# Performance work log

Hardware: AMD Instinct MI355X
Metric: run time of the kernel (lower is better)

The kernel has to match this reference:

```python
import jax, jax.numpy as jnp
import numpy as np

LN_EPS = 1e-5
ADJ_EPS = 1e-8
LRELU_SLOPE = 0.2


def _layernorm(x, g, b):
    m = x.mean(-1, keepdims=True)
    v = ((x - m) ** 2).mean(-1, keepdims=True)
    return (x - m) / jnp.sqrt(v + LN_EPS) * g + b


def _gat(h, adj, W, a, dim_head, proj=None):
    # h: [B,N,Din]; adj: [B,N,N]; W: [Din, H*dh]; a: [H, 2*dh]
    B, N, _ = h.shape
    H = a.shape[0]
    ht = (h @ W).reshape(B, N, H, dim_head)          # [B,N,H,dh]
    # additive attention: a . [h_i || h_j] splits into two rank-1 terms,
    # so we never materialize the O(B N^2 H 2dh) concat tensor.
    ei = jnp.einsum('bnhd,hd->bnh', ht, a[:, :dim_head])
    ej = jnp.einsum('bnhd,hd->bnh', ht, a[:, dim_head:])
    e = ei[:, :, None, :] + ej[:, None, :, :]        # [B,N,N,H]
    e = jnp.where(e > 0, e, LRELU_SLOPE * e)         # leaky relu(0.2)
    mask = (adj > 0)[..., None]                      # [B,N,N,1]
    e = jnp.where(mask, e, -jnp.inf)
    alpha = jax.nn.softmax(e, axis=2)                # softmax over neighbors m
    hagg = jnp.einsum('bnmh,bmhd->bnhd', alpha, ht)  # [B,N,H,dh]
    out = hagg.reshape(B, N, -1)
    if proj is not None:
        Wp, bp = proj
        out = out @ Wp + bp
    return out


def setup_inputs() -> dict:
    key = jax.random.key(0)
    ks = jax.random.split(key, 24)
    B, N, DN, DH, H = 64, 360, 360, 256, 8
    s = 0.05
    nrm = lambda k, sh, sc=s: (jax.random.normal(k, sh) * sc).astype(jnp.float32)
    return {
        'mind_matrix': jax.random.uniform(ks[0], (B, N, N), dtype=jnp.float32),
        'roi_features_img': jax.random.normal(ks[1], (B, N, DH), dtype=jnp.float32),
        'group_prior': jax.random.uniform(ks[2], (N, N), dtype=jnp.float32),
        'Wnp': nrm(ks[3], (DN, DH)), 'bnp': jnp.zeros((DH,), jnp.float32),
        'Wrf': nrm(ks[4], (2 * DH, DH)), 'brf': jnp.zeros((DH,), jnp.float32),
        'ln_g': jnp.ones((DH,), jnp.float32), 'ln_b': jnp.zeros((DH,), jnp.float32),
        'Wp1': nrm(ks[5], (1, 32)), 'bp1': jnp.zeros((32,), jnp.float32),
        'Wp2': nrm(ks[6], (32, 1)), 'bp2': jnp.zeros((1,), jnp.float32),
        'gatW0': nrm(ks[7], (DH, DH)), 'gata0': nrm(ks[8], (H, 64), 1.0),
        'gatW1': nrm(ks[9], (DH, DH)), 'gata1': nrm(ks[10], (H, 64), 1.0),
        'gatW2': nrm(ks[11], (DH, H * DH)), 'gata2': nrm(ks[12], (H, 2 * DH), 1.0),
        'projW': nrm(ks[13], (H * DH, DH)), 'projb': jnp.zeros((DH,), jnp.float32),
        'Wr1': nrm(ks[14], (DH, DH)), 'br1': jnp.zeros((DH,), jnp.float32),
        'Wr2': nrm(ks[15], (DH, DH)), 'br2': jnp.zeros((DH,), jnp.float32),
    }


def reference(mind_matrix, roi_features_img, group_prior,
              Wnp, bnp, Wrf, brf, ln_g, ln_b,
              Wp1, bp1, Wp2, bp2,
              gatW0, gata0, gatW1, gata1, gatW2, gata2, projW, projb,
              Wr1, br1, Wr2, br2):
    # node feature fusion
    node_mind = mind_matrix @ Wnp + bnp                       # [B,N,256]
    nf = jnp.concatenate([node_mind, roi_features_img], -1) @ Wrf + brf
    nf = jax.nn.gelu(_layernorm(nf, ln_g, ln_b), approximate=False)
    # prior-modulated adjacency (tau = 1.0)
    adj_base = jnp.exp(-mind_matrix)                          # [B,N,N]
    pm = jax.nn.relu(group_prior[..., None] @ Wp1 + bp1)      # [N,N,32]
    pm = jax.nn.sigmoid(pm @ Wp2 + bp2)[..., 0]               # [N,N]
    adj_mod = adj_base * (1.0 + pm)[None]
    adj_norm = adj_mod / (adj_mod.sum(-1, keepdims=True) + ADJ_EPS)
    # hierarchical GAT (dropout inactive at eval)
    h = _gat(nf, adj_norm, gatW0, gata0, 32)
    h = _gat(h, adj_norm, gatW1, gata1, 32)
    h = _gat(h, adj_norm, gatW2, gata2, 256, (projW, projb))  # concat=False layer
    # attention readout
    node_attention = jax.nn.softmax(jnp.linalg.norm(h, axis=-1), axis=-1)  # [B,N]
    ge = jnp.einsum('bn,bnd->bd', node_attention, h)
    ge = jax.nn.gelu(ge @ Wr1 + br1, approximate=False) @ Wr2 + br2
    return ge, h, node_attention
```

## Files before the change

### kernel.cpp

```cpp
#include <hip/hip_runtime.h>
#include <hip/hip_bf16.h>
#include <math.h>


#define B_ 64
#define N_ 360
#define D_ 256
#define H_ 8
#define ROWS_ (B_ * N_)
#define CHUNK01 30
#define SCPAD 964

__device__ __forceinline__ float gelu_f(float x) {
    return 0.5f * x * (1.f + erff(x * 0.70710678118654752440f));
}

__global__ __launch_bounds__(256) void gemm_tiled(
    const float* __restrict__ A1, const float* __restrict__ B1, int K1, int lda1, int ldb1,
    const float* __restrict__ A2, const float* __restrict__ B2, int K2, int lda2, int ldb2,
    const float* __restrict__ bias, float* __restrict__ C, int M, int N, int ldc,
    size_t sA, size_t sB, size_t sC)
{
    __shared__ float As[2][32][132];
    __shared__ float Bs[2][32][64];
    const int tid = threadIdx.x;
    const int z = blockIdx.z;
    const int bm = blockIdx.y * 128;
    const int bn = blockIdx.x * 64;
    const int tr = (tid >> 4) * 8;
    const int tc = (tid & 15) * 4;
    const int lar = tid >> 3;
    const int lak = (tid & 7) * 4;
    const int lbk = tid >> 4;
    const int lbc = (tid & 15) * 4;

    float acc[8][4] = {};
    float4 rA[4], rB[2];

    for (int pass = 0; pass < 2; ++pass) {
        const float* Ab = pass ? A2 : A1;
        const float* Bb = pass ? B2 : B1;
        if (Ab == nullptr) continue;
        const float* A  = Ab + (pass ? (size_t)0 : (size_t)z * sA);
        const float* Bm = Bb + (pass ? (size_t)0 : (size_t)z * sB);
        const int K   = pass ? K2 : K1;
        const int lda = pass ? lda2 : lda1;
        const int ldb = pass ? ldb2 : ldb1;
        const int S = (K + 31) >> 5;

        auto loadA = [&](int s) {
            const int k0 = s << 5;
            #pragma unroll
            for (int j = 0; j < 4; ++j) {
                const int gr = bm + lar + j * 32;
                const int gk = k0 + lak;
                float4 v; v.x = v.y = v.z = v.w = 0.f;
                if (gr < M) {
                    if (gk + 3 < K) {
                        v = *(const float4*)&A[(size_t)gr * lda + gk];
                    } else {
                        float t0 = 0.f, t1 = 0.f, t2 = 0.f, t3 = 0.f;
                        if (gk + 0 < K) t0 = A[(size_t)gr * lda + gk + 0];
                        if (gk + 1 < K) t1 = A[(size_t)gr * lda + gk + 1];
                        if (gk + 2 < K) t2 = A[(size_t)gr * lda + gk + 2];
                        if (gk + 3 < K) t3 = A[(size_t)gr * lda + gk + 3];
                        v.x = t0; v.y = t1; v.z = t2; v.w = t3;
                    }
                }
                rA[j] = v;
            }
        };
        auto loadB = [&](int s) {
            const int k0 = s << 5;
            #pragma unroll
            for (int j = 0; j < 2; ++j) {
                const int gk = k0 + lbk + j * 16;
                float4 v; v.x = v.y = v.z = v.w = 0.f;
                if (gk < K) v = *(const float4*)&Bm[(size_t)gk * ldb + bn + lbc];
                rB[j] = v;
            }
        };
        auto storeA = [&](int buf) {
            #pragma unroll
            for (int j = 0; j < 4; ++j) {
                const int row = lar + j * 32;
                As[buf][lak + 0][row] = rA[j].x;
                As[buf][lak + 1][row] = rA[j].y;
                As[buf][lak + 2][row] = rA[j].z;
                As[buf][lak + 3][row] = rA[j].w;
            }
        };
        auto storeB = [&](int buf) {
            #pragma unroll
            for (int j = 0; j < 2; ++j)
                *(float4*)&Bs[buf][lbk + j * 16][lbc] = rB[j];
        };

        loadA(0); loadB(0);
        storeA(0); storeB(0);
        __syncthreads();
        for (int s = 0; s < S; ++s) {
            const int cur = s & 1;
            if (s + 1 < S) { loadA(s + 1); loadB(s + 1); }
            #pragma unroll
            for (int k = 0; k < 32; ++k) {
                const float4 a0 = *(const float4*)&As[cur][k][tr];
                const float4 a1 = *(const float4*)&As[cur][k][tr + 4];
                const float4 bv = *(const float4*)&Bs[cur][k][tc];
                const float av[8] = {a0.x, a0.y, a0.z, a0.w, a1.x, a1.y, a1.z, a1.w};
                const float bb[4] = {bv.x, bv.y, bv.z, bv.w};
                #pragma unroll
                for (int i = 0; i < 8; ++i)
                    #pragma unroll
                    for (int j = 0; j < 4; ++j)
                        acc[i][j] += av[i] * bb[j];
            }
            if (s + 1 < S) { storeA(cur ^ 1); storeB(cur ^ 1); }
            __syncthreads();
        }
    }

    float4 bz; bz.x = bz.y = bz.z = bz.w = 0.f;
    if (bias) bz = *(const float4*)&bias[bn + tc];
    float* Cz = C + (size_t)z * sC;
    #pragma unroll
    for (int i = 0; i < 8; ++i) {
        const int r = bm + tr + i;
        if (r < M) {
            float4 o;
            o.x = acc[i][0] + bz.x;
            o.y = acc[i][1] + bz.y;
            o.z = acc[i][2] + bz.z;
            o.w = acc[i][3] + bz.w;
            *(float4*)&Cz[(size_t)r * ldc + bn + tc] = o;
        }
    }
}

__global__ __launch_bounds__(256) void biascomb_kernel(
    const float* __restrict__ bnp, const float* __restrict__ Wrf,
    const float* __restrict__ brf, float* __restrict__ bcomb)
{
    int c = threadIdx.x;
    float acc = brf[c];
    for (int k = 0; k < 256; ++k) acc += bnp[k] * Wrf[k * 256 + c];
    bcomb[c] = acc;
}

__global__ __launch_bounds__(256) void uv_kernel(
    const float* __restrict__ gatW2, const float* __restrict__ a2,
    float* __restrict__ u, float* __restrict__ v)
{
    const int h = blockIdx.x;
    const int i = threadIdx.x;
    const float* wrow = gatW2 + (size_t)i * 2048 + h * 256;
    const float* ai = a2 + h * 512;
    float su = 0.f, sv = 0.f;
    for (int j = 0; j < 256; ++j) {
        float w = wrow[j];
        su += w * ai[j];
        sv += w * ai[256 + j];
    }
    u[h * 256 + i] = su;
    v[h * 256 + i] = sv;
}

__global__ __launch_bounds__(64) void ln_gelu_kernel(
    float* __restrict__ x, const float* __restrict__ g, const float* __restrict__ b)
{
    const size_t row = blockIdx.x;
    const int t = threadIdx.x;
    float4 v = *(const float4*)&x[row * 256 + t * 4];
    float s = v.x + v.y + v.z + v.w;
    #pragma unroll
    for (int m = 1; m < 64; m <<= 1) s += __shfl_xor(s, m);
    float mean = s * (1.f / 256.f);
    float dx = v.x - mean, dy = v.y - mean, dz = v.z - mean, dw = v.w - mean;
    float q = dx * dx + dy * dy + dz * dz + dw * dw;
    #pragma unroll
    for (int m = 1; m < 64; m <<= 1) q += __shfl_xor(q, m);
    float rstd = 1.f / sqrtf(q * (1.f / 256.f) + 1e-5f);
    float4 gg = *(const float4*)&g[t * 4];
    float4 bb = *(const float4*)&b[t * 4];
    float4 r;
    r.x = gelu_f(dx * rstd * gg.x + bb.x);
    r.y = gelu_f(dy * rstd * gg.y + bb.y);
    r.z = gelu_f(dz * rstd * gg.z + bb.z);
    r.w = gelu_f(dw * rstd * gg.w + bb.w);
    *(float4*)&x[row * 256 + t * 4] = r;
}

template <int DH>
__global__ __launch_bounds__(64) void eiej_kernel(
    const float* __restrict__ ht, const float* __restrict__ a,
    float* __restrict__ ei, float* __restrict__ ej)
{
    const size_t row = blockIdx.x;
    const int t = threadIdx.x;
    constexpr int E = (H_ * DH) / 64;
    const int h = t >> 3;
    const int d0 = (t & 7) * E;
    const float* hp = ht + row * (H_ * DH) + h * DH + d0;
    const float* ap = a + h * 2 * DH + d0;
    float se = 0.f, sj = 0.f;
    #pragma unroll
    for (int i = 0; i < E; i += 4) {
        float4 x = *(const float4*)&hp[i];
        float4 u = *(const float4*)&ap[i];
        float4 w = *(const float4*)&ap[DH + i];
        se += x.x * u.x + x.y * u.y + x.z * u.z + x.w * u.w;
        sj += x.x * w.x + x.y * w.y + x.z * w.z + x.w * w.w;
    }
    se += __shfl_xor(se, 1); sj += __shfl_xor(sj, 1);
    se += __shfl_xor(se, 2); sj += __shfl_xor(sj, 2);
    se += __shfl_xor(se, 4); sj += __shfl_xor(sj, 4);
    if ((t & 7) == 0) {
        ei[row * H_ + h] = se;
        ej[row * H_ + h] = sj;
    }
}

__global__ __launch_bounds__(64) void eiej2_kernel(
    const float* __restrict__ h2, const float* __restrict__ u,
    const float* __restrict__ v, float* __restrict__ ei, float* __restrict__ ej)
{
    const size_t row = blockIdx.x;
    const int t = threadIdx.x;
    const int h = t >> 3;
    const int d0 = (t & 7) * 32;
    const float* hp = h2 + row * 256 + d0;
    const float* up = u + h * 256 + d0;
    const float* vp = v + h * 256 + d0;
    float se = 0.f, sj = 0.f;
    #pragma unroll
    for (int i = 0; i < 32; i += 4) {
        float4 x = *(const float4*)&hp[i];
        float4 uu = *(const float4*)&up[i];
        float4 vv = *(const float4*)&vp[i];
        se += x.x * uu.x + x.y * uu.y + x.z * uu.z + x.w * uu.w;
        sj += x.x * vv.x + x.y * vv.y + x.z * vv.z + x.w * vv.w;
    }
    se += __shfl_xor(se, 1); sj += __shfl_xor(sj, 1);
    se += __shfl_xor(se, 2); sj += __shfl_xor(sj, 2);
    se += __shfl_xor(se, 4); sj += __shfl_xor(sj, 4);
    if ((t & 7) == 0) {
        ei[row * H_ + h] = se;
        ej[row * H_ + h] = sj;
    }
}

__global__ __launch_bounds__(256) void gat01_agg(
    const float* __restrict__ ht, const float* __restrict__ ei,
    const float* __restrict__ ej, float* __restrict__ out)
{
    __shared__ float scT[8 * SCPAD];
    __shared__ float ejs[8][N_];
    __shared__ float eis[8][32];
    __shared__ float rinv_s[8][32];
    __shared__ float maxej_s[8];
    const int tid = threadIdx.x;
    const int b = blockIdx.y;
    const int n0 = blockIdx.x * 32;
    const int nrows = min(32, N_ - n0);

    for (int idx = tid; idx < N_ * H_; idx += 256) {
        const int m = idx >> 3, h = idx & 7;
        ejs[h][m] = ej[(size_t)(b * N_ + m) * H_ + h];
    }
    const int ph = tid >> 5, pr = tid & 31;
    eis[ph][pr] = (pr < nrows) ? ei[(size_t)(b * N_ + n0 + pr) * H_ + ph] : 0.f;
    __syncthreads();

    {
        float mx = -1e30f;
        for (int m = pr; m < N_; m += 32) mx = fmaxf(mx, ejs[ph][m]);
        mx = fmaxf(mx, __shfl_xor(mx, 1));
        mx = fmaxf(mx, __shfl_xor(mx, 2));
        mx = fmaxf(mx, __shfl_xor(mx, 4));
        mx = fmaxf(mx, __shfl_xor(mx, 8));
        mx = fmaxf(mx, __shfl_xor(mx, 16));
        if (pr == 0) maxej_s[ph] = mx;
    }
    __syncthreads();

    const float ei_r = eis[ph][pr];
    float mrow = ei_r + maxej_s[ph];
    mrow = mrow > 0.f ? mrow : 0.2f * mrow;
    float rsum = 0.f;

    const int rg = tid >> 5, cg = tid & 31;
    const int vh = cg >> 2;
    const float* Vp = ht + (size_t)b * N_ * D_ + cg * 8;
    float acc[4][8] = {};

    for (int c0 = 0; c0 < N_; c0 += CHUNK01) {
        float* sp = scT + ph * SCPAD + pr;
        #pragma unroll 6
        for (int mm = 0; mm < CHUNK01; ++mm) {
            float e = ei_r + ejs[ph][c0 + mm];
            e = e > 0.f ? e : 0.2f * e;
            float p = __expf(e - mrow);
            sp[mm * 32] = p;
            rsum += p;
        }
        __syncthreads();
        const float* st = scT + vh * SCPAD + rg * 4;
        #pragma unroll 2
        for (int mm = 0; mm < CHUNK01; ++mm) {
            const int m = c0 + mm;
            const float4 a4 = *(const float4*)&st[mm * 32];
            const float4 v0 = *(const float4*)&Vp[(size_t)m * D_];
            const float4 v1 = *(const float4*)&Vp[(size_t)m * D_ + 4];
            const float a[4] = {a4.x, a4.y, a4.z, a4.w};
            const float v[8] = {v0.x, v0.y, v0.z, v0.w, v1.x, v1.y, v1.z, v1.w};
            #pragma unroll
            for (int i = 0; i < 4; ++i)
                #pragma unroll
                for (int j = 0; j < 8; ++j)
                    acc[i][j] += a[i] * v[j];
        }
        __syncthreads();
    }

    rinv_s[ph][pr] = 1.f / rsum;
    __syncthreads();

    #pragma unroll
    for (int i = 0; i < 4; ++i) {
        const int r = rg * 4 + i;
        if (r < nrows) {
            const float ri = rinv_s[vh][r];
            float* op = out + (size_t)(b * N_ + n0 + r) * D_ + cg * 8;
            float4 o0, o1;
            o0.x = acc[i][0] * ri; o0.y = acc[i][1] * ri;
            o0.z = acc[i][2] * ri; o0.w = acc[i][3] * ri;
            o1.x = acc[i][4] * ri; o1.y = acc[i][5] * ri;
            o1.z = acc[i][6] * ri; o1.w = acc[i][7] * ri;
            *(float4*)&op[0] = o0;
            *(float4*)&op[4] = o1;
        }
    }
}

__global__ __launch_bounds__(256) void gat2_agg4(
    const float* __restrict__ Zbase, size_t zstride,
    const float* __restrict__ ei, const float* __restrict__ ej,
    const float* __restrict__ projb, float* __restrict__ out,
    int hbase, int first)
{
    __shared__ float scT[N_][32];
    __shared__ float ejs[N_];
    __shared__ float eis[32];
    __shared__ float psum[8][32];
    __shared__ float rinv_s[32];
    __shared__ float red4[4];
    const int tid = threadIdx.x;
    const int b = blockIdx.y;
    const int n0 = blockIdx.x * 32;
    const int nrows = min(32, N_ - n0);
    const int rg = tid >> 5, cg = tid & 31;
    const int sr = tid & 31, sub = tid >> 5;
    float acc[4][8] = {};

    for (int hh = 0; hh < 4; ++hh) {
        const int h = hbase + hh;
        for (int m = tid; m < N_; m += 256) ejs[m] = ej[(size_t)(b * N_ + m) * H_ + h];
        if (tid < 32) eis[tid] = (tid < nrows) ? ei[(size_t)(b * N_ + n0 + tid) * H_ + h] : 0.f;
        __syncthreads();

        float mx = -1e30f;
        for (int m = tid; m < N_; m += 256) mx = fmaxf(mx, ejs[m]);
        #pragma unroll
        for (int s = 1; s < 64; s <<= 1) mx = fmaxf(mx, __shfl_xor(mx, s));
        if ((tid & 63) == 0) red4[tid >> 6] = mx;
        __syncthreads();
        const float maxej = fmaxf(fmaxf(red4[0], red4[1]), fmaxf(red4[2], red4[3]));

        const float ei_r = eis[sr];
        float mrow = ei_r + maxej;
        mrow = mrow > 0.f ? mrow : 0.2f * mrow;

        float s = 0.f;
        for (int m = sub; m < N_; m += 8) {
            float e = ei_r + ejs[m];
            e = e > 0.f ? e : 0.2f * e;
            s += __expf(e - mrow);
        }
        psum[sub][sr] = s;
        __syncthreads();
        if (tid < 32) {
            float t = psum[0][tid] + psum[1][tid] + psum[2][tid] + psum[3][tid]
                    + psum[4][tid] + psum[5][tid] + psum[6][tid] + psum[7][tid];
            rinv_s[tid] = 1.f / t;
        }
        __syncthreads();
        const float ri = rinv_s[sr];
        for (int m = sub; m < N_; m += 8) {
            float e = ei_r + ejs[m];
            e = e > 0.f ? e : 0.2f * e;
            scT[m][sr] = __expf(e - mrow) * ri;
        }
        __syncthreads();

        const float* Vp = Zbase + (size_t)hh * zstride + (size_t)b * N_ * D_ + cg * 8;
        #pragma unroll 2
        for (int m = 0; m < N_; ++m) {
            const float4 a4 = *(const float4*)&scT[m][rg * 4];
            const float4 v0 = *(const float4*)&Vp[(size_t)m * D_];
            const float4 v1 = *(const float4*)&Vp[(size_t)m * D_ + 4];
            const float a[4] = {a4.x, a4.y, a4.z, a4.w};
            const float v[8] = {v0.x, v0.y, v0.z, v0.w, v1.x, v1.y, v1.z, v1.w};
            #pragma unroll
            for (int i = 0; i < 4; ++i)
                #pragma unroll
                for (int j = 0; j < 8; ++j)
                    acc[i][j] += a[i] * v[j];
        }
        __syncthreads();
    }

    #pragma unroll
    for (int i = 0; i < 4; ++i) {
        const int r = rg * 4 + i;
        if (r < nrows) {
            float* op = out + (size_t)(b * N_ + n0 + r) * D_ + cg * 8;
            if (first) {
                const float4 p0 = *(const float4*)&projb[cg * 8];
                const float4 p1 = *(const float4*)&projb[cg * 8 + 4];
                float4 o0, o1;
                o0.x = acc[i][0] + p0.x; o0.y = acc[i][1] + p0.y;
                o0.z = acc[i][2] + p0.z; o0.w = acc[i][3] + p0.w;
                o1.x = acc[i][4] + p1.x; o1.y = acc[i][5] + p1.y;
                o1.z = acc[i][6] + p1.z; o1.w = acc[i][7] + p1.w;
                *(float4*)&op[0] = o0;
                *(float4*)&op[4] = o1;
            } else {
                float4 o0 = *(const float4*)&op[0];
                float4 o1 = *(const float4*)&op[4];
                o0.x += acc[i][0]; o0.y += acc[i][1];
                o0.z += acc[i][2]; o0.w += acc[i][3];
                o1.x += acc[i][4]; o1.y += acc[i][5];
                o1.z += acc[i][6]; o1.w += acc[i][7];
                *(float4*)&op[0] = o0;
                *(float4*)&op[4] = o1;
            }
        }
    }
}

__global__ __launch_bounds__(64) void rownorm_kernel(
    const float* __restrict__ h, float* __restrict__ nrm)
{
    const size_t row = blockIdx.x;
    const int t = threadIdx.x;
    float4 v = *(const float4*)&h[row * 256 + t * 4];
    float s = v.x * v.x + v.y * v.y + v.z * v.z + v.w * v.w;
    #pragma unroll
    for (int m = 1; m < 64; m <<= 1) s += __shfl_xor(s, m);
    if (t == 0) nrm[row] = sqrtf(s);
}

__global__ __launch_bounds__(64) void softmax_n_kernel(
    const float* __restrict__ nrm, float* __restrict__ attn)
{
    const int b = blockIdx.x;
    const int t = threadIdx.x;
    float v[6];
    float mx = -1e30f;
    #pragma unroll
    for (int i = 0; i < 6; ++i) {
        int m = t + i * 64;
        v[i] = (m < N_) ? nrm[b * N_ + m] : -1e30f;
        mx = fmaxf(mx, v[i]);
    }
    #pragma unroll
    for (int m = 1; m < 64; m <<= 1) mx = fmaxf(mx, __shfl_xor(mx, m));
    float s = 0.f;
    #pragma unroll
    for (int i = 0; i < 6; ++i) {
        int m = t + i * 64;
        float p = (m < N_) ? __expf(v[i] - mx) : 0.f;
        v[i] = p;
        s += p;
    }
    #pragma unroll
    for (int m = 1; m < 64; m <<= 1) s += __shfl_xor(s, m);
    const float inv = 1.f / s;
    #pragma unroll
    for (int i = 0; i < 6; ++i) {
        int m = t + i * 64;
        if (m < N_) attn[b * N_ + m] = v[i] * inv;
    }
}

__global__ __launch_bounds__(256) void ge_kernel(
    const float* __restrict__ attn, const float* __restrict__ h, float* __restrict__ ge)
{
    __shared__ float a[N_];
    const int b = blockIdx.x;
    const int t = threadIdx.x;
    for (int m = t; m < N_; m += 256) a[m] = attn[b * N_ + m];
    __syncthreads();
    float acc = 0.f;
    const float* hp = h + (size_t)b * N_ * 256 + t;
    for (int m = 0; m < N_; ++m) acc += a[m] * hp[(size_t)m * 256];
    ge[b * 256 + t] = acc;
}

__global__ __launch_bounds__(256) void mlp_kernel(
    const float* __restrict__ X, const float* __restrict__ W,
    const float* __restrict__ bias, float* __restrict__ Y, int applyGelu)
{
    __shared__ float xs[256];
    const int b = blockIdx.x;
    const int t = threadIdx.x;
    xs[t] = X[b * 256 + t];
    __syncthreads();
    float acc = bias[t];
    for (int k = 0; k < 256; ++k) acc += xs[k] * W[k * 256 + t];
    if (applyGelu) acc = gelu_f(acc);
    Y[b * 256 + t] = acc;
}


extern "C" void kernel_launch(void* const* d_in, const int* in_sizes, int n_in,
                              void* d_out, int out_size, void* d_ws, size_t ws_size,
                              hipStream_t stream) {
    const float* mind  = (const float*)d_in[0];
    const float* roi   = (const float*)d_in[1];
    const float* Wnp   = (const float*)d_in[3];
    const float* bnp   = (const float*)d_in[4];
    const float* Wrf   = (const float*)d_in[5];
    const float* brf   = (const float*)d_in[6];
    const float* ln_g  = (const float*)d_in[7];
    const float* ln_b  = (const float*)d_in[8];
    const float* gatW0 = (const float*)d_in[13];
    const float* gata0 = (const float*)d_in[14];
    const float* gatW1 = (const float*)d_in[15];
    const float* gata1 = (const float*)d_in[16];
    const float* gatW2 = (const float*)d_in[17];
    const float* gata2 = (const float*)d_in[18];
    const float* projW = (const float*)d_in[19];
    const float* projb = (const float*)d_in[20];
    const float* Wr1   = (const float*)d_in[21];
    const float* br1   = (const float*)d_in[22];
    const float* Wr2   = (const float*)d_in[23];
    const float* br2   = (const float*)d_in[24];

    const size_t SZ = (size_t)ROWS_ * D_;
    float* ws = (float*)d_ws;
    float* s0 = ws;
    float* s1 = ws + SZ;
    float* s2 = ws + 2 * SZ;
    float* s3 = ws + 3 * SZ;
    float* s4 = ws + 4 * SZ;
    float* tail  = ws + 5 * SZ;
    float* ei_b  = tail;
    float* ej_b  = ei_b + (size_t)ROWS_ * H_;
    float* Wcomb = ej_b + (size_t)ROWS_ * H_;
    float* bcomb = Wcomb + 360 * 256;
    float* Gbuf  = bcomb + 256;
    float* uvec  = Gbuf + 8 * 256 * 256;
    float* vvec  = uvec + 8 * 256;
    float* norms = vvec + 8 * 256;
    float* ge0   = norms + ROWS_;
    float* ge1   = ge0 + B_ * D_;

    const size_t need = (size_t)(ge1 + B_ * D_ - ws) * sizeof(float);
    if (ws_size < need) return;

    float* out    = (float*)d_out;
    float* out_ge = out;
    float* out_h  = out + (size_t)B_ * D_;
    float* out_at = out_h + (size_t)ROWS_ * D_;

    const dim3 blk(256);

    gemm_tiled<<<dim3(4, 3), blk, 0, stream>>>(
        Wnp, Wrf, 256, 256, 256,
        nullptr, nullptr, 0, 0, 0,
        nullptr, Wcomb, 360, 256, 256, 0, 0, 0);
    biascomb_kernel<<<1, 256, 0, stream>>>(bnp, Wrf, brf, bcomb);
    gemm_tiled<<<dim3(4, 180), blk, 0, stream>>>(
        mind, Wcomb, 360, 360, 256,
        roi, Wrf + 256 * 256, 256, 256, 256,
        bcomb, s1, ROWS_, 256, 256, 0, 0, 0);
    ln_gelu_kernel<<<ROWS_, 64, 0, stream>>>(s1, ln_g, ln_b);

    gemm_tiled<<<dim3(4, 180), blk, 0, stream>>>(
        s1, gatW0, 256, 256, 256,
        nullptr, nullptr, 0, 0, 0,
        nullptr, s2, ROWS_, 256, 256, 0, 0, 0);
    eiej_kernel<32><<<ROWS_, 64, 0, stream>>>(s2, gata0, ei_b, ej_b);
    gat01_agg<<<dim3(12, B_), blk, 0, stream>>>(s2, ei_b, ej_b, s3);

    gemm_tiled<<<dim3(4, 180), blk, 0, stream>>>(
        s3, gatW1, 256, 256, 256,
        nullptr, nullptr, 0, 0, 0,
        nullptr, s2, ROWS_, 256, 256, 0, 0, 0);
    eiej_kernel<32><<<ROWS_, 64, 0, stream>>>(s2, gata1, ei_b, ej_b);
    gat01_agg<<<dim3(12, B_), blk, 0, stream>>>(s2, ei_b, ej_b, s0);

    gemm_tiled<<<dim3(4, 2, 8), blk, 0, stream>>>(
        gatW2, projW, 256, 2048, 256,
        nullptr, nullptr, 0, 0, 0,
        nullptr, Gbuf, 256, 256, 256,
        256, (size_t)256 * 256, (size_t)256 * 256);
    uv_kernel<<<8, 256, 0, stream>>>(gatW2, gata2, uvec, vvec);
    eiej2_kernel<<<ROWS_, 64, 0, stream>>>(s0, uvec, vvec, ei_b, ej_b);

    gemm_tiled<<<dim3(4, 180, 4), blk, 0, stream>>>(
        s0, Gbuf, 256, 256, 256,
        nullptr, nullptr, 0, 0, 0,
        nullptr, s1, ROWS_, 256, 256,
        0, (size_t)256 * 256, SZ);
    gat2_agg4<<<dim3(12, B_), blk, 0, stream>>>(
        s1, SZ, ei_b, ej_b, projb, out_h, 0, 1);
    gemm_tiled<<<dim3(4, 180, 4), blk, 0, stream>>>(
        s0, Gbuf + (size_t)4 * 256 * 256, 256, 256, 256,
        nullptr, nullptr, 0, 0, 0,
        nullptr, s1, ROWS_, 256, 256,
        0, (size_t)256 * 256, SZ);
    gat2_agg4<<<dim3(12, B_), blk, 0, stream>>>(
        s1, SZ, ei_b, ej_b, projb, out_h, 4, 0);

    rownorm_kernel<<<ROWS_, 64, 0, stream>>>(out_h, norms);
    softmax_n_kernel<<<B_, 64, 0, stream>>>(norms, out_at);
    ge_kernel<<<B_, 256, 0, stream>>>(out_at, out_h, ge0);
    mlp_kernel<<<B_, 256, 0, stream>>>(ge0, Wr1, br1, ge1, 1);
    mlp_kernel<<<B_, 256, 0, stream>>>(ge1, Wr2, br2, out_ge, 0);
}
```

Before: 2.048 ms.

## Repartition GAT aggregation blocks by column slice instead of row tile

The GAT aggregation kernels now give each block all 360 query rows for one 32-column slice (one head in layers 0/1, one output slice in layer 2), instead of 32 rows across all 256 columns. Each V row is therefore read once per block rather than once per row tile, and the softmax denominator is accumulated alongside the weighted sum, which removes the separate sum pass in the layer-2 kernel. The trade-offs are fewer blocks (8x64 instead of 12x64), 16 of 256 threads idle in the accumulate loop, and more accumulator registers (6x8 per thread, plus a second 6x8 set in the layer-2 kernel).

```diff
diff --git a/kernel.cpp b/kernel.cpp
--- a/kernel.cpp
+++ b/kernel.cpp
@@ -8,8 +8,8 @@
 #define D_ 256
 #define H_ 8
 #define ROWS_ (B_ * N_)
-#define CHUNK01 30
-#define SCPAD 964
+#define CH 32
+#define SCST 368
 
 __device__ __forceinline__ float gelu_f(float x) {
     return 0.5f * x * (1.f + erff(x * 0.70710678118654752440f));
@@ -249,88 +249,84 @@
     }
 }
 
-__global__ __launch_bounds__(256) void gat01_agg(
+__global__ __launch_bounds__(256) void gat01_aggC(
     const float* __restrict__ ht, const float* __restrict__ ei,
     const float* __restrict__ ej, float* __restrict__ out)
 {
-    __shared__ float scT[8 * SCPAD];
-    __shared__ float ejs[8][N_];
-    __shared__ float eis[8][32];
-    __shared__ float rinv_s[8][32];
-    __shared__ float maxej_s[8];
+    __shared__ float scT[CH][SCST];
+    __shared__ float ejs[N_], eis[N_], mrow_s[N_];
+    __shared__ float red4[4];
     const int tid = threadIdx.x;
+    const int h = blockIdx.x;
     const int b = blockIdx.y;
-    const int n0 = blockIdx.x * 32;
-    const int nrows = min(32, N_ - n0);
-
-    for (int idx = tid; idx < N_ * H_; idx += 256) {
-        const int m = idx >> 3, h = idx & 7;
-        ejs[h][m] = ej[(size_t)(b * N_ + m) * H_ + h];
-    }
-    const int ph = tid >> 5, pr = tid & 31;
-    eis[ph][pr] = (pr < nrows) ? ei[(size_t)(b * N_ + n0 + pr) * H_ + ph] : 0.f;
+
+    for (int r = tid; r < N_; r += 256) {
+        ejs[r] = ej[(size_t)(b * N_ + r) * H_ + h];
+        eis[r] = ei[(size_t)(b * N_ + r) * H_ + h];
+    }
     __syncthreads();
-
-    {
-        float mx = -1e30f;
-        for (int m = pr; m < N_; m += 32) mx = fmaxf(mx, ejs[ph][m]);
-        mx = fmaxf(mx, __shfl_xor(mx, 1));
-        mx = fmaxf(mx, __shfl_xor(mx, 2));
-        mx = fmaxf(mx, __shfl_xor(mx, 4));
-        mx = fmaxf(mx, __shfl_xor(mx, 8));
-        mx = fmaxf(mx, __shfl_xor(mx, 16));
-        if (pr == 0) maxej_s[ph] = mx;
-    }
+    float mx = -1e30f;
+    for (int m = tid; m < N_; m += 256) mx = fmaxf(mx, ejs[m]);
+    #pragma unroll
+    for (int s = 1; s < 64; s <<= 1) mx = fmaxf(mx, __shfl_xor(mx, s));
+    if ((tid & 63) == 0) red4[tid >> 6] = mx;
     __syncthreads();
-
-    const float ei_r = eis[ph][pr];
-    float mrow = ei_r + maxej_s[ph];
-    mrow = mrow > 0.f ? mrow : 0.2f * mrow;
-    float rsum = 0.f;
-
-    const int rg = tid >> 5, cg = tid & 31;
-    const int vh = cg >> 2;
-    const float* Vp = ht + (size_t)b * N_ * D_ + cg * 8;
-    float acc[4][8] = {};
-
-    for (int c0 = 0; c0 < N_; c0 += CHUNK01) {
-        float* sp = scT + ph * SCPAD + pr;
-        #pragma unroll 6
-        for (int mm = 0; mm < CHUNK01; ++mm) {
-            float e = ei_r + ejs[ph][c0 + mm];
-            e = e > 0.f ? e : 0.2f * e;
-            float p = __expf(e - mrow);
-            sp[mm * 32] = p;
-            rsum += p;
+    const float maxej = fmaxf(fmaxf(red4[0], red4[1]), fmaxf(red4[2], red4[3]));
+    for (int r = tid; r < N_; r += 256) {
+        float t = eis[r] + maxej;
+        mrow_s[r] = t > 0.f ? t : 0.2f * t;
+    }
+    __syncthreads();
+
+    const int smm = tid >> 3, srs = tid & 7;
+    const int cg = tid & 3, rg = tid >> 2;
+    const float* Vp = ht + (size_t)b * N_ * D_ + h * 32 + cg * 8;
+    float acc[6][8] = {};
+    float rsum[6] = {};
+
+    for (int c0 = 0; c0 < N_; c0 += CH) {
+        const int mcnt = min(CH, N_ - c0);
+        if (smm < mcnt) {
+            const float ejv = ejs[c0 + smm];
+            float* sp = &scT[smm][srs * 45];
+            const float* ep = &eis[srs * 45];
+            const float* mp = &mrow_s[srs * 45];
+            #pragma unroll 5
+            for (int i = 0; i < 45; ++i) {
+                float e = ep[i] + ejv;
+                e = e > 0.f ? e : 0.2f * e;
+                sp[i] = __expf(e - mp[i]);
+            }
         }
         __syncthreads();
-        const float* st = scT + vh * SCPAD + rg * 4;
-        #pragma unroll 2
-        for (int mm = 0; mm < CHUNK01; ++mm) {
-            const int m = c0 + mm;
-            const float4 a4 = *(const float4*)&st[mm * 32];
-            const float4 v0 = *(const float4*)&Vp[(size_t)m * D_];
-            const float4 v1 = *(const float4*)&Vp[(size_t)m * D_ + 4];
-            const float a[4] = {a4.x, a4.y, a4.z, a4.w};
-            const float v[8] = {v0.x, v0.y, v0.z, v0.w, v1.x, v1.y, v1.z, v1.w};
-            #pragma unroll
-            for (int i = 0; i < 4; ++i)
+        if (rg < 60) {
+            for (int mm = 0; mm < mcnt; ++mm) {
+                const float2 a0 = *(const float2*)&scT[mm][rg * 6 + 0];
+                const float2 a1 = *(const float2*)&scT[mm][rg * 6 + 2];
+                const float2 a2 = *(const float2*)&scT[mm][rg * 6 + 4];
+                const float a[6] = {a0.x, a0.y, a1.x, a1.y, a2.x, a2.y};
+                const size_t mo = (size_t)(c0 + mm) * D_;
+                const float4 v0 = *(const float4*)&Vp[mo];
+                const float4 v1 = *(const float4*)&Vp[mo + 4];
+                const float v[8] = {v0.x, v0.y, v0.z, v0.w, v1.x, v1.y, v1.z, v1.w};
                 #pragma unroll
-                for (int j = 0; j < 8; ++j)
-                    acc[i][j] += a[i] * v[j];
+                for (int i = 0; i < 6; ++i) {
+                    rsum[i] += a[i];
+                    #pragma unroll
+                    for (int j = 0; j < 8; ++j)
+                        acc[i][j] += a[i] * v[j];
+                }
+            }
         }
         __syncthreads();
     }
 
-    rinv_s[ph][pr] = 1.f / rsum;
-    __syncthreads();
-
-    #pragma unroll
-    for (int i = 0; i < 4; ++i) {
-        const int r = rg * 4 + i;
-        if (r < nrows) {
-            const float ri = rinv_s[vh][r];
-            float* op = out + (size_t)(b * N_ + n0 + r) * D_ + cg * 8;
+    if (rg < 60) {
+        #pragma unroll
+        for (int i = 0; i < 6; ++i) {
+            const int r = rg * 6 + i;
+            const float ri = 1.f / rsum[i];
+            float* op = out + (size_t)(b * N_ + r) * D_ + h * 32 + cg * 8;
             float4 o0, o1;
             o0.x = acc[i][0] * ri; o0.y = acc[i][1] * ri;
             o0.z = acc[i][2] * ri; o0.w = acc[i][3] * ri;
@@ -342,32 +338,29 @@
     }
 }
 
-__global__ __launch_bounds__(256) void gat2_agg4(
+__global__ __launch_bounds__(256) void gat2_aggC4(
     const float* __restrict__ Zbase, size_t zstride,
     const float* __restrict__ ei, const float* __restrict__ ej,
     const float* __restrict__ projb, float* __restrict__ out,
     int hbase, int first)
 {
-    __shared__ float scT[N_][32];
-    __shared__ float ejs[N_];
-    __shared__ float eis[32];
-    __shared__ float psum[8][32];
-    __shared__ float rinv_s[32];
+    __shared__ float scT[CH][SCST];
+    __shared__ float ejs[N_], eis[N_], mrow_s[N_];
     __shared__ float red4[4];
     const int tid = threadIdx.x;
+    const int cslice = blockIdx.x;
     const int b = blockIdx.y;
-    const int n0 = blockIdx.x * 32;
-    const int nrows = min(32, N_ - n0);
-    const int rg = tid >> 5, cg = tid & 31;
-    const int sr = tid & 31, sub = tid >> 5;
-    float acc[4][8] = {};
+    const int smm = tid >> 3, srs = tid & 7;
+    const int cg = tid & 3, rg = tid >> 2;
+    float acc[6][8] = {};
 
     for (int hh = 0; hh < 4; ++hh) {
         const int h = hbase + hh;
-        for (int m = tid; m < N_; m += 256) ejs[m] = ej[(size_t)(b * N_ + m) * H_ + h];
-        if (tid < 32) eis[tid] = (tid < nrows) ? ei[(size_t)(b * N_ + n0 + tid) * H_ + h] : 0.f;
+        for (int r = tid; r < N_; r += 256) {
+            ejs[r] = ej[(size_t)(b * N_ + r) * H_ + h];
+            eis[r] = ei[(size_t)(b * N_ + r) * H_ + h];
+        }
         __syncthreads();
-
         float mx = -1e30f;
         for (int m = tid; m < N_; m += 256) mx = fmaxf(mx, ejs[m]);
         #pragma unroll
@@ -375,58 +368,74 @@
         if ((tid & 63) == 0) red4[tid >> 6] = mx;
         __syncthreads();
         const float maxej = fmaxf(fmaxf(red4[0], red4[1]), fmaxf(red4[2], red4[3]));
-
-        const float ei_r = eis[sr];
-        float mrow = ei_r + maxej;
-        mrow = mrow > 0.f ? mrow : 0.2f * mrow;
-
-        float s = 0.f;
-        for (int m = sub; m < N_; m += 8) {
-            float e = ei_r + ejs[m];
-            e = e > 0.f ? e : 0.2f * e;
-            s += __expf(e - mrow);
-        }
-        psum[sub][sr] = s;
+        for (int r = tid; r < N_; r += 256) {
+            float t = eis[r] + maxej;
+            mrow_s[r] = t > 0.f ? t : 0.2f * t;
+        }
         __syncthreads();
-        if (tid < 32) {
-            float t = psum[0][tid] + psum[1][tid] + psum[2][tid] + psum[3][tid]
-                    + psum[4][tid] + psum[5][tid] + psum[6][tid] + psum[7][tid];
-            rinv_s[tid] = 1.f / t;
-        }
-        __syncthreads();
-        const float ri = rinv_s[sr];
-        for (int m = sub; m < N_; m += 8) {
-            float e = ei_r + ejs[m];
-            e = e > 0.f ? e : 0.2f * e;
-            scT[m][sr] = __expf(e - mrow) * ri;
-        }
-        __syncthreads();
-
-        const float* Vp = Zbase + (size_t)hh * zstride + (size_t)b * N_ * D_ + cg * 8;
-        #pragma unroll 2
-        for (int m = 0; m < N_; ++m) {
-            const float4 a4 = *(const float4*)&scT[m][rg * 4];
-            const float4 v0 = *(const float4*)&Vp[(size_t)m * D_];
-            const float4 v1 = *(const float4*)&Vp[(size_t)m * D_ + 4];
-            const float a[4] = {a4.x, a4.y, a4.z, a4.w};
-            const float v[8] = {v0.x, v0.y, v0.z, v0.w, v1.x, v1.y, v1.z, v1.w};
+
+        const float* Vp = Zbase + (size_t)hh * zstride
+                        + (size_t)b * N_ * D_ + cslice * 32 + cg * 8;
+        float acc_h[6][8] = {};
+        float rsum[6] = {};
+
+        for (int c0 = 0; c0 < N_; c0 += CH) {
+            const int mcnt = min(CH, N_ - c0);
+            if (smm < mcnt) {
+                const float ejv = ejs[c0 + smm];
+                float* sp = &scT[smm][srs * 45];
+                const float* ep = &eis[srs * 45];
+                const float* mp = &mrow_s[srs * 45];
+                #pragma unroll 5
+                for (int i = 0; i < 45; ++i) {
+                    float e = ep[i] + ejv;
+                    e = e > 0.f ? e : 0.2f * e;
+                    sp[i] = __expf(e - mp[i]);
+                }
+            }
+            __syncthreads();
+            if (rg < 60) {
+                for (int mm = 0; mm < mcnt; ++mm) {
+                    const float2 a0 = *(const float2*)&scT[mm][rg * 6 + 0];
+                    const float2 a1 = *(const float2*)&scT[mm][rg * 6 + 2];
+                    const float2 a2 = *(const float2*)&scT[mm][rg * 6 + 4];
+                    const float a[6] = {a0.x, a0.y, a1.x, a1.y, a2.x, a2.y};
+                    const size_t mo = (size_t)(c0 + mm) * D_;
+                    const float4 v0 = *(const float4*)&Vp[mo];
+                    const float4 v1 = *(const float4*)&Vp[mo + 4];
+                    const float v[8] = {v0.x, v0.y, v0.z, v0.w, v1.x, v1.y, v1.z, v1.w};
+                    #pragma unroll
+                    for (int i = 0; i < 6; ++i) {
+                        rsum[i] += a[i];
+                        #pragma unroll
+                        for (int j = 0; j < 8; ++j)
+                            acc_h[i][j] += a[i] * v[j];
+                    }
+                }
+            }
+            __syncthreads();
+        }
+
+        if (rg < 60) {
             #pragma unroll
-            for (int i = 0; i < 4; ++i)
+            for (int i = 0; i < 6; ++i) {
+                const float ri = 1.f / rsum[i];
                 #pragma unroll
                 for (int j = 0; j < 8; ++j)
-                    acc[i][j] += a[i] * v[j];
+                    acc[i][j] += acc_h[i][j] * ri;
+            }
         }
         __syncthreads();
     }
 
-    #pragma unroll
-    for (int i = 0; i < 4; ++i) {
-        const int r = rg * 4 + i;
-        if (r < nrows) {
-            float* op = out + (size_t)(b * N_ + n0 + r) * D_ + cg * 8;
+    if (rg < 60) {
+        #pragma unroll
+        for (int i = 0; i < 6; ++i) {
+            const int r = rg * 6 + i;
+            float* op = out + (size_t)(b * N_ + r) * D_ + cslice * 32 + cg * 8;
             if (first) {
-                const float4 p0 = *(const float4*)&projb[cg * 8];
-                const float4 p1 = *(const float4*)&projb[cg * 8 + 4];
+                const float4 p0 = *(const float4*)&projb[cslice * 32 + cg * 8];
+                const float4 p1 = *(const float4*)&projb[cslice * 32 + cg * 8 + 4];
                 float4 o0, o1;
                 o0.x = acc[i][0] + p0.x; o0.y = acc[i][1] + p0.y;
                 o0.z = acc[i][2] + p0.z; o0.w = acc[i][3] + p0.w;
@@ -592,14 +601,14 @@
         nullptr, nullptr, 0, 0, 0,
         nullptr, s2, ROWS_, 256, 256, 0, 0, 0);
     eiej_kernel<32><<<ROWS_, 64, 0, stream>>>(s2, gata0, ei_b, ej_b);
-    gat01_agg<<<dim3(12, B_), blk, 0, stream>>>(s2, ei_b, ej_b, s3);
+    gat01_aggC<<<dim3(H_, B_), blk, 0, stream>>>(s2, ei_b, ej_b, s3);
 
     gemm_tiled<<<dim3(4, 180), blk, 0, stream>>>(
         s3, gatW1, 256, 256, 256,
         nullptr, nullptr, 0, 0, 0,
         nullptr, s2, ROWS_, 256, 256, 0, 0, 0);
     eiej_kernel<32><<<ROWS_, 64, 0, stream>>>(s2, gata1, ei_b, ej_b);
-    gat01_agg<<<dim3(12, B_), blk, 0, stream>>>(s2, ei_b, ej_b, s0);
+    gat01_aggC<<<dim3(H_, B_), blk, 0, stream>>>(s2, ei_b, ej_b, s0);
 
     gemm_tiled<<<dim3(4, 2, 8), blk, 0, stream>>>(
         gatW2, projW, 256, 2048, 256,
@@ -614,14 +623,14 @@
         nullptr, nullptr, 0, 0, 0,
         nullptr, s1, ROWS_, 256, 256,
         0, (size_t)256 * 256, SZ);
-    gat2_agg4<<<dim3(12, B_), blk, 0, stream>>>(
+    gat2_aggC4<<<dim3(8, B_), blk, 0, stream>>>(
         s1, SZ, ei_b, ej_b, projb, out_h, 0, 1);
     gemm_tiled<<<dim3(4, 180, 4), blk, 0, stream>>>(
         s0, Gbuf + (size_t)4 * 256 * 256, 256, 256, 256,
         nullptr, nullptr, 0, 0, 0,
         nullptr, s1, ROWS_, 256, 256,
         0, (size_t)256 * 256, SZ);
-    gat2_agg4<<<dim3(12, B_), blk, 0, stream>>>(
+    gat2_aggC4<<<dim3(8, B_), blk, 0, stream>>>(
         s1, SZ, ei_b, ej_b, projb, out_h, 4, 0);
 
     rownorm_kernel<<<ROWS_, 64, 0, stream>>>(out_h, norms);
```

Result: slower. 2.613 ms (+27.6%).
